# Optimization experiments

Measured on AMD Instinct MI355X. Metric: run time of the kernel, lower is better.

## Reference

```python
import jax, jax.numpy as jnp
import numpy as np

P, Q, R, H1, H2, PH, B = 32, 32, 8, 128, 64, 16, 8192
PAIRS = P * Q
OUT = PAIRS * R  # X_Z_layer output units


def _pairwise_mask(p, q, r):
    # rows i*q+k correspond to pair (x_i, z_k): connected to x_i and z_k only
    mx = np.zeros((p * q, p), np.float32)
    for i in range(p):
        mx[i * q:(i + 1) * q, i] = 1.0
    mz = np.tile(np.eye(q, dtype=np.float32), (p, 1))
    m = np.concatenate([mx, mz], axis=1)          # [p*q, p+q]
    return np.repeat(m, r, axis=0)                 # [p*q*r, p+q]


def setup_inputs() -> dict:
    key = jax.random.key(0)
    ks = jax.random.split(key, 24)
    rn = lambda k, s, sc=0.1: jax.random.normal(k, s, jnp.float32) * sc
    x = jax.random.normal(ks[0], (B, P), jnp.float32)
    z = jax.random.normal(ks[1], (B, Q), jnp.float32)
    # X_mlp: P -> H1 -> H2 -> 1
    xw1, xb1 = rn(ks[2], (P, H1)), rn(ks[3], (H1,))
    xw2, xb2 = rn(ks[4], (H1, H2)), rn(ks[5], (H2,))
    xw3, xb3 = rn(ks[6], (H2, 1)), rn(ks[7], (1,))
    # Z_mlp: Q -> H1 -> H2 -> 1
    zw1, zb1 = rn(ks[8], (Q, H1)), rn(ks[9], (H1,))
    zw2, zb2 = rn(ks[10], (Q if False else H1, H2)), rn(ks[11], (H2,))
    zw3, zb3 = rn(ks[12], (H2, 1)), rn(ks[13], (1,))
    # masked X_Z_layer: weight pre-multiplied by structured mask (as in __init__)
    mask = jnp.asarray(_pairwise_mask(P, Q, R))    # [OUT, P+Q]
    xzw = (rn(ks[14], (OUT, P + Q)) * mask).T      # [P+Q, OUT]
    xzb = rn(ks[15], (OUT,))
    # 1024 tiny per-pair MLPs: R -> PH (bias) -> 1 (no bias), stacked
    pw1 = rn(ks[16], (PAIRS, R, PH))
    pb1 = rn(ks[17], (PAIRS, PH))
    pw2 = rn(ks[18], (PAIRS, PH))
    return dict(x=x, z=z, xw1=xw1, xb1=xb1, xw2=xw2, xb2=xb2, xw3=xw3, xb3=xb3,
                zw1=zw1, zb1=zb1, zw2=zw2, zb2=zb2, zw3=zw3, zb3=zb3,
                xzw=xzw, xzb=xzb, pw1=pw1, pb1=pb1, pw2=pw2)


def reference(x, z, xw1, xb1, xw2, xb2, xw3, xb3,
              zw1, zb1, zw2, zb2, zw3, zb3, xzw, xzb, pw1, pb1, pw2):
    relu = jax.nn.relu
    # main-effect MLPs
    hx = relu(relu(x @ xw1 + xb1) @ xw2 + xb2)
    out_x = hx @ xw3 + xb3                         # [B,1]
    hz = relu(relu(z @ zw1 + zb1) @ zw2 + zb2)
    out_z = hz @ zw3 + zb3                         # [B,1]
    # masked interaction layer
    xz = jnp.concatenate([x, z], axis=1)           # [B, P+Q]
    h = relu(xz @ xzw + xzb)                       # [B, OUT]
    # all 1024 per-pair MLPs as one batched GEMM
    hp = h.reshape(h.shape[0], PAIRS, R)           # [B, pairs, R]
    t = relu(jnp.einsum('bpr,prh->bph', hp, pw1) + pb1)
    out_xz = jnp.einsum('bph,ph->b', t, pw2)[:, None]  # sum over pairs -> [B,1]
    return out_x + out_z + out_xz
```

## Files before the change

### kernel.cpp

```cpp
#include <hip/hip_runtime.h>

#define B_TOT 8192
#define PP 32
#define QQ 32
#define RR 8
#define H1 128
#define H2 64
#define PHH 16
#define PAIRS 1024
#define OUT_UNITS 8192

#define NBLK_IA 4096
#define NBLK_MM 512

typedef float f32x16 __attribute__((ext_vector_type(16)));
typedef short s16x8  __attribute__((ext_vector_type(8)));

union FragU { s16x8 v; unsigned int u[4]; };

__device__ inline unsigned int pack_bf16(float lo, float hi) {
    return __builtin_amdgcn_perm(__float_as_uint(hi), __float_as_uint(lo), 0x07060302u);
}

union SharedU {
    struct {
        float zT[16][128];
        float4 lwx[16][2];
        float4 lwz[16][2];
        float4 lhb[16][2];
        unsigned lpw1[16][4][16];
        float lpb[16][16];
        float lpw2[16][16];
        float red[128][33];
    } ia;
    struct {
        float h1T[128][65];
        float red2[4][64];
    } mm;
};

__global__ __launch_bounds__(256, 4) void fused_k(
    const float* __restrict__ x, const float* __restrict__ z,
    const float* __restrict__ xw1, const float* __restrict__ xb1,
    const float* __restrict__ xw2, const float* __restrict__ xb2,
    const float* __restrict__ xw3, const float* __restrict__ xb3,
    const float* __restrict__ zw1, const float* __restrict__ zb1,
    const float* __restrict__ zw2, const float* __restrict__ zb2,
    const float* __restrict__ zw3, const float* __restrict__ zb3,
    const float* __restrict__ xzw, const float* __restrict__ xzb,
    const float* __restrict__ pw1, const float* __restrict__ pb1,
    const float* __restrict__ pw2, float* __restrict__ out)
{
    __shared__ SharedU sh;
    const int bid  = blockIdx.x;
    const int t    = threadIdx.x;
    const int w    = t >> 6;
    const int lane = t & 63;

    if (bid < NBLK_IA) {
        const int bx    = bid & 63;
        const int y     = bid >> 6;
        const int m     = lane & 31;
        const int kh    = lane >> 5;
        const int jj    = m & 15;
        const int cph   = m >> 4;
        const int b0    = bx * 128;
        const int i_x   = y >> 1;
        const int k0    = (y & 1) * 16;
        const int pair0 = y * 16;

        {
            int row = t >> 1;
            int c8  = (t & 1) * 8;
            const float* src = z + (size_t)(b0 + row) * 32 + k0 + c8;
            float4 a4 = *reinterpret_cast<const float4*>(src);
            float4 b4 = *reinterpret_cast<const float4*>(src + 4);
            sh.ia.zT[c8+0][row] = a4.x; sh.ia.zT[c8+1][row] = a4.y;
            sh.ia.zT[c8+2][row] = a4.z; sh.ia.zT[c8+3][row] = a4.w;
            sh.ia.zT[c8+4][row] = b4.x; sh.ia.zT[c8+5][row] = b4.y;
            sh.ia.zT[c8+6][row] = b4.z; sh.ia.zT[c8+7][row] = b4.w;
        }
        if (t < 128) {
            int p = t >> 3, c = t & 7;
            int gp = pair0 + p;
            reinterpret_cast<float*>(sh.ia.lwx)[t] = xzw[(size_t)i_x * OUT_UNITS + gp*8 + c];
            reinterpret_cast<float*>(sh.ia.lwz)[t] = xzw[(size_t)(32 + k0 + p) * OUT_UNITS + gp*8 + c];
            reinterpret_cast<float*>(sh.ia.lhb)[t] = xzb[gp*8 + c];
        }
        {
            int p = t >> 4, j = t & 15;
            int gp = pair0 + p;
            sh.ia.lpb[p][j]  = pb1[gp*PHH + j];
            sh.ia.lpw2[p][j] = pw2[gp*PHH + j];
        }
        #pragma unroll
        for (int it = 0; it < 4; ++it) {
            int idx = t + it * 256;
            int p = idx >> 6, u = (idx >> 4) & 3, j = idx & 15;
            int gp = pair0 + p;
            float lo = pw1[(size_t)gp * 128 + (2*u)*16 + j];
            float hi = pw1[(size_t)gp * 128 + (2*u+1)*16 + j];
            sh.ia.lpw1[p][u][j] = pack_bf16(lo, hi);
        }

        const int bl = (w & 1) * 64 + m;
        const float xv0 = x[(size_t)(b0 + bl)      * 32 + i_x];
        const float xv1 = x[(size_t)(b0 + bl + 32) * 32 + i_x];
        __syncthreads();

        f32x16 acc0, acc1;
        #pragma unroll
        for (int r = 0; r < 16; ++r) { acc0[r] = 0.f; acc1[r] = 0.f; }

        const bool realB = (kh == cph);
        const int  ppl0  = (w >> 1) * 4;

        #pragma unroll 2
        for (int kk = 0; kk < 4; ++kk) {
            const int ppl = ppl0 + kk;
            const int pAl = 2*ppl + kh;
            const int pBl = 2*ppl + cph;

            const float zv0 = sh.ia.zT[pAl][bl];
            const float zv1 = sh.ia.zT[pAl][bl + 32];
            const float4 wxa = sh.ia.lwx[pAl][0], wxb = sh.ia.lwx[pAl][1];
            const float4 wza = sh.ia.lwz[pAl][0], wzb = sh.ia.lwz[pAl][1];
            const float4 hba = sh.ia.lhb[pAl][0], hbb = sh.ia.lhb[pAl][1];

            float h0[8], h1v[8];
            h0[0] = fmaxf(fmaf(xv0, wxa.x, fmaf(zv0, wza.x, hba.x)), 0.f);
            h0[1] = fmaxf(fmaf(xv0, wxa.y, fmaf(zv0, wza.y, hba.y)), 0.f);
            h0[2] = fmaxf(fmaf(xv0, wxa.z, fmaf(zv0, wza.z, hba.z)), 0.f);
            h0[3] = fmaxf(fmaf(xv0, wxa.w, fmaf(zv0, wza.w, hba.w)), 0.f);
            h0[4] = fmaxf(fmaf(xv0, wxb.x, fmaf(zv0, wzb.x, hbb.x)), 0.f);
            h0[5] = fmaxf(fmaf(xv0, wxb.y, fmaf(zv0, wzb.y, hbb.y)), 0.f);
            h0[6] = fmaxf(fmaf(xv0, wxb.z, fmaf(zv0, wzb.z, hbb.z)), 0.f);
            h0[7] = fmaxf(fmaf(xv0, wxb.w, fmaf(zv0, wzb.w, hbb.w)), 0.f);
            h1v[0] = fmaxf(fmaf(xv1, wxa.x, fmaf(zv1, wza.x, hba.x)), 0.f);
            h1v[1] = fmaxf(fmaf(xv1, wxa.y, fmaf(zv1, wza.y, hba.y)), 0.f);
            h1v[2] = fmaxf(fmaf(xv1, wxa.z, fmaf(zv1, wza.z, hba.z)), 0.f);
            h1v[3] = fmaxf(fmaf(xv1, wxa.w, fmaf(zv1, wza.w, hba.w)), 0.f);
            h1v[4] = fmaxf(fmaf(xv1, wxb.x, fmaf(zv1, wzb.x, hbb.x)), 0.f);
            h1v[5] = fmaxf(fmaf(xv1, wxb.y, fmaf(zv1, wzb.y, hbb.y)), 0.f);
            h1v[6] = fmaxf(fmaf(xv1, wxb.z, fmaf(zv1, wzb.z, hbb.z)), 0.f);
            h1v[7] = fmaxf(fmaf(xv1, wxb.w, fmaf(zv1, wzb.w, hbb.w)), 0.f);

            FragU a0, a1, bf;
            a0.u[0] = pack_bf16(h0[0], h0[1]);
            a0.u[1] = pack_bf16(h0[2], h0[3]);
            a0.u[2] = pack_bf16(h0[4], h0[5]);
            a0.u[3] = pack_bf16(h0[6], h0[7]);
            a1.u[0] = pack_bf16(h1v[0], h1v[1]);
            a1.u[1] = pack_bf16(h1v[2], h1v[3]);
            a1.u[2] = pack_bf16(h1v[4], h1v[5]);
            a1.u[3] = pack_bf16(h1v[6], h1v[7]);
            bf.u[0] = realB ? sh.ia.lpw1[pBl][0][jj] : 0u;
            bf.u[1] = realB ? sh.ia.lpw1[pBl][1][jj] : 0u;
            bf.u[2] = realB ? sh.ia.lpw1[pBl][2][jj] : 0u;
            bf.u[3] = realB ? sh.ia.lpw1[pBl][3][jj] : 0u;

            const float pbv = sh.ia.lpb[pBl][jj];
            const float w2v = sh.ia.lpw2[pBl][jj];

            f32x16 cpb;
            #pragma unroll
            for (int r = 0; r < 16; ++r) cpb[r] = pbv;

            f32x16 d0 = __builtin_amdgcn_mfma_f32_32x32x16_bf16(a0.v, bf.v, cpb, 0, 0, 0);
            f32x16 d1 = __builtin_amdgcn_mfma_f32_32x32x16_bf16(a1.v, bf.v, cpb, 0, 0, 0);

            #pragma unroll
            for (int r = 0; r < 16; ++r)
                acc0[r] = fmaf(fmaxf(d0[r], 0.f), w2v, acc0[r]);
            #pragma unroll
            for (int r = 0; r < 16; ++r)
                acc1[r] = fmaf(fmaxf(d1[r], 0.f), w2v, acc1[r]);
        }

        const int rb0 = (w & 1) * 64;
        if (w < 2) {
            #pragma unroll
            for (int r = 0; r < 16; ++r) {
                int rowf = (r & 3) + 8 * (r >> 2) + 4 * kh;
                sh.ia.red[rb0 + rowf][m]      = acc0[r];
                sh.ia.red[rb0 + 32 + rowf][m] = acc1[r];
            }
        }
        __syncthreads();
        if (w >= 2) {
            #pragma unroll
            for (int r = 0; r < 16; ++r) {
                int rowf = (r & 3) + 8 * (r >> 2) + 4 * kh;
                sh.ia.red[rb0 + rowf][m]      += acc0[r];
                sh.ia.red[rb0 + 32 + rowf][m] += acc1[r];
            }
        }
        __syncthreads();
        if (t < 128) {
            float s = 0.f;
            #pragma unroll
            for (int c = 0; c < 32; ++c) s += sh.ia.red[t][c];
            atomicAdd(out + b0 + t, s);
        }
    } else {
        const int r2    = bid - NBLK_IA;
        const int btile = r2 & 127;
        const int hf    = (r2 >> 7) & 1;
        const int which = (r2 >> 8) & 1;
        const float* in = which ? z   : x;
        const float* w1 = which ? zw1 : xw1;
        const float* b1 = which ? zb1 : xb1;
        const float* w2 = which ? zw2 : xw2;
        const float* b2 = which ? zb2 : xb2;
        const float* w3 = which ? zw3 : xw3;
        const float* b3 = which ? zb3 : xb3;

        const int wu = __builtin_amdgcn_readfirstlane(w);
        const int b0 = btile * 64;

        float xr[32];
        const float4* xrp = reinterpret_cast<const float4*>(in + (size_t)(b0 + lane) * 32);
        #pragma unroll
        for (int q = 0; q < 8; ++q) {
            float4 v = xrp[q];
            xr[4*q] = v.x; xr[4*q+1] = v.y; xr[4*q+2] = v.z; xr[4*q+3] = v.w;
        }

        float h1[32];
        #pragma unroll
        for (int j = 0; j < 32; ++j) h1[j] = b1[wu*32 + j];
        #pragma unroll
        for (int mm = 0; mm < 32; ++mm) {
            float xv = xr[mm];
            #pragma unroll
            for (int j = 0; j < 32; ++j)
                h1[j] = fmaf(xv, w1[mm*H1 + wu*32 + j], h1[j]);
        }
        #pragma unroll
        for (int j = 0; j < 32; ++j)
            sh.mm.h1T[wu*32 + j][lane] = fmaxf(h1[j], 0.f);
        __syncthreads();

        const int n0 = __builtin_amdgcn_readfirstlane(hf*32 + wu*8);
        float h2[8];
        #pragma unroll
        for (int n = 0; n < 8; ++n) h2[n] = b2[n0 + n];
        #pragma unroll 4
        for (int mm = 0; mm < 128; ++mm) {
            float hv = sh.mm.h1T[mm][lane];
            #pragma unroll
            for (int n = 0; n < 8; ++n)
                h2[n] = fmaf(hv, w2[mm*H2 + n0 + n], h2[n]);
        }
        float p = 0.f;
        #pragma unroll
        for (int n = 0; n < 8; ++n)
            p = fmaf(fmaxf(h2[n], 0.f), w3[n0 + n], p);

        sh.mm.red2[wu][lane] = p;
        __syncthreads();
        if (wu == 0) {
            float s = sh.mm.red2[0][lane] + sh.mm.red2[1][lane]
                    + sh.mm.red2[2][lane] + sh.mm.red2[3][lane];
            if (hf == 0) s += b3[0];
            atomicAdd(out + b0 + lane, s);
        }
    }
}

extern "C" void kernel_launch(void* const* d_in, const int* in_sizes, int n_in,
                              void* d_out, int out_size, void* d_ws, size_t ws_size,
                              hipStream_t stream) {
    const float* x   = (const float*)d_in[0];
    const float* z   = (const float*)d_in[1];
    const float* xw1 = (const float*)d_in[2];
    const float* xb1 = (const float*)d_in[3];
    const float* xw2 = (const float*)d_in[4];
    const float* xb2 = (const float*)d_in[5];
    const float* xw3 = (const float*)d_in[6];
    const float* xb3 = (const float*)d_in[7];
    const float* zw1 = (const float*)d_in[8];
    const float* zb1 = (const float*)d_in[9];
    const float* zw2 = (const float*)d_in[10];
    const float* zb2 = (const float*)d_in[11];
    const float* zw3 = (const float*)d_in[12];
    const float* zb3 = (const float*)d_in[13];
    const float* xzw = (const float*)d_in[14];
    const float* xzb = (const float*)d_in[15];
    const float* pw1 = (const float*)d_in[16];
    const float* pb1 = (const float*)d_in[17];
    const float* pw2 = (const float*)d_in[18];
    float* out = (float*)d_out;

    hipMemsetAsync(out, 0, (size_t)out_size * sizeof(float), stream);

    fused_k<<<dim3(NBLK_IA + NBLK_MM), 256, 0, stream>>>(
        x, z, xw1, xb1, xw2, xb2, xw3, xb3,
        zw1, zb1, zw2, zb2, zw3, zb3,
        xzw, xzb, pw1, pb1, pw2, out);
}
```

Baseline: 137.4 us.

## Shrink shared memory footprint and raise occupancy; schedule MLP blocks first

The interaction-stage reduction buffer now overlays the staging arrays through a nested union, with an extra barrier before the overlay is written. The main-effect MLP path computes its hidden layer in two halves of 64 units, halving the h1T buffer and the h1 register array. Launch bounds rise from 4 to 6 blocks per SM so that smaller LDS and register use can allow more resident blocks. The heavier MLP blocks move to the low block indices so they are dispatched first rather than trailing at the tail. The changes add extra barriers and risk register pressure or spills under the tighter launch bound.

```diff
diff --git a/kernel.cpp b/kernel.cpp
--- a/kernel.cpp
+++ b/kernel.cpp
@@ -23,23 +23,25 @@
 }
 
 union SharedU {
-    struct {
-        float zT[16][128];
-        float4 lwx[16][2];
-        float4 lwz[16][2];
-        float4 lhb[16][2];
-        unsigned lpw1[16][4][16];
-        float lpb[16][16];
-        float lpw2[16][16];
+    union {
+        struct {
+            float zT[16][128];
+            float4 lwx[16][2];
+            float4 lwz[16][2];
+            float4 lhb[16][2];
+            unsigned lpw1[16][4][16];
+            float lpb[16][16];
+            float lpw2[16][16];
+        } s;
         float red[128][33];
     } ia;
     struct {
-        float h1T[128][65];
+        float h1T[64][65];
         float red2[4][64];
     } mm;
 };
 
-__global__ __launch_bounds__(256, 4) void fused_k(
+__global__ __launch_bounds__(256, 6) void fused_k(
     const float* __restrict__ x, const float* __restrict__ z,
     const float* __restrict__ xw1, const float* __restrict__ xb1,
     const float* __restrict__ xw2, const float* __restrict__ xb2,
@@ -57,9 +59,10 @@
     const int w    = t >> 6;
     const int lane = t & 63;
 
-    if (bid < NBLK_IA) {
-        const int bx    = bid & 63;
-        const int y     = bid >> 6;
+    if (bid >= NBLK_MM) {
+        const int ib    = bid - NBLK_MM;
+        const int bx    = ib & 63;
+        const int y     = ib >> 6;
         const int m     = lane & 31;
         const int kh    = lane >> 5;
         const int jj    = m & 15;
@@ -75,23 +78,23 @@
             const float* src = z + (size_t)(b0 + row) * 32 + k0 + c8;
             float4 a4 = *reinterpret_cast<const float4*>(src);
             float4 b4 = *reinterpret_cast<const float4*>(src + 4);
-            sh.ia.zT[c8+0][row] = a4.x; sh.ia.zT[c8+1][row] = a4.y;
-            sh.ia.zT[c8+2][row] = a4.z; sh.ia.zT[c8+3][row] = a4.w;
-            sh.ia.zT[c8+4][row] = b4.x; sh.ia.zT[c8+5][row] = b4.y;
-            sh.ia.zT[c8+6][row] = b4.z; sh.ia.zT[c8+7][row] = b4.w;
+            sh.ia.s.zT[c8+0][row] = a4.x; sh.ia.s.zT[c8+1][row] = a4.y;
+            sh.ia.s.zT[c8+2][row] = a4.z; sh.ia.s.zT[c8+3][row] = a4.w;
+            sh.ia.s.zT[c8+4][row] = b4.x; sh.ia.s.zT[c8+5][row] = b4.y;
+            sh.ia.s.zT[c8+6][row] = b4.z; sh.ia.s.zT[c8+7][row] = b4.w;
         }
         if (t < 128) {
             int p = t >> 3, c = t & 7;
             int gp = pair0 + p;
-            reinterpret_cast<float*>(sh.ia.lwx)[t] = xzw[(size_t)i_x * OUT_UNITS + gp*8 + c];
-            reinterpret_cast<float*>(sh.ia.lwz)[t] = xzw[(size_t)(32 + k0 + p) * OUT_UNITS + gp*8 + c];
-            reinterpret_cast<float*>(sh.ia.lhb)[t] = xzb[gp*8 + c];
+            reinterpret_cast<float*>(sh.ia.s.lwx)[t] = xzw[(size_t)i_x * OUT_UNITS + gp*8 + c];
+            reinterpret_cast<float*>(sh.ia.s.lwz)[t] = xzw[(size_t)(32 + k0 + p) * OUT_UNITS + gp*8 + c];
+            reinterpret_cast<float*>(sh.ia.s.lhb)[t] = xzb[gp*8 + c];
         }
         {
             int p = t >> 4, j = t & 15;
             int gp = pair0 + p;
-            sh.ia.lpb[p][j]  = pb1[gp*PHH + j];
-            sh.ia.lpw2[p][j] = pw2[gp*PHH + j];
+            sh.ia.s.lpb[p][j]  = pb1[gp*PHH + j];
+            sh.ia.s.lpw2[p][j] = pw2[gp*PHH + j];
         }
         #pragma unroll
         for (int it = 0; it < 4; ++it) {
@@ -100,7 +103,7 @@
             int gp = pair0 + p;
             float lo = pw1[(size_t)gp * 128 + (2*u)*16 + j];
             float hi = pw1[(size_t)gp * 128 + (2*u+1)*16 + j];
-            sh.ia.lpw1[p][u][j] = pack_bf16(lo, hi);
+            sh.ia.s.lpw1[p][u][j] = pack_bf16(lo, hi);
         }
 
         const int bl = (w & 1) * 64 + m;
@@ -121,11 +124,11 @@
             const int pAl = 2*ppl + kh;
             const int pBl = 2*ppl + cph;
 
-            const float zv0 = sh.ia.zT[pAl][bl];
-            const float zv1 = sh.ia.zT[pAl][bl + 32];
-            const float4 wxa = sh.ia.lwx[pAl][0], wxb = sh.ia.lwx[pAl][1];
-            const float4 wza = sh.ia.lwz[pAl][0], wzb = sh.ia.lwz[pAl][1];
-            const float4 hba = sh.ia.lhb[pAl][0], hbb = sh.ia.lhb[pAl][1];
+            const float zv0 = sh.ia.s.zT[pAl][bl];
+            const float zv1 = sh.ia.s.zT[pAl][bl + 32];
+            const float4 wxa = sh.ia.s.lwx[pAl][0], wxb = sh.ia.s.lwx[pAl][1];
+            const float4 wza = sh.ia.s.lwz[pAl][0], wzb = sh.ia.s.lwz[pAl][1];
+            const float4 hba = sh.ia.s.lhb[pAl][0], hbb = sh.ia.s.lhb[pAl][1];
 
             float h0[8], h1v[8];
             h0[0] = fmaxf(fmaf(xv0, wxa.x, fmaf(zv0, wza.x, hba.x)), 0.f);
@@ -154,13 +157,13 @@
             a1.u[1] = pack_bf16(h1v[2], h1v[3]);
             a1.u[2] = pack_bf16(h1v[4], h1v[5]);
             a1.u[3] = pack_bf16(h1v[6], h1v[7]);
-            bf.u[0] = realB ? sh.ia.lpw1[pBl][0][jj] : 0u;
-            bf.u[1] = realB ? sh.ia.lpw1[pBl][1][jj] : 0u;
-            bf.u[2] = realB ? sh.ia.lpw1[pBl][2][jj] : 0u;
-            bf.u[3] = realB ? sh.ia.lpw1[pBl][3][jj] : 0u;
-
-            const float pbv = sh.ia.lpb[pBl][jj];
-            const float w2v = sh.ia.lpw2[pBl][jj];
+            bf.u[0] = realB ? sh.ia.s.lpw1[pBl][0][jj] : 0u;
+            bf.u[1] = realB ? sh.ia.s.lpw1[pBl][1][jj] : 0u;
+            bf.u[2] = realB ? sh.ia.s.lpw1[pBl][2][jj] : 0u;
+            bf.u[3] = realB ? sh.ia.s.lpw1[pBl][3][jj] : 0u;
+
+            const float pbv = sh.ia.s.lpb[pBl][jj];
+            const float w2v = sh.ia.s.lpw2[pBl][jj];
 
             f32x16 cpb;
             #pragma unroll
@@ -177,6 +180,7 @@
                 acc1[r] = fmaf(fmaxf(d1[r], 0.f), w2v, acc1[r]);
         }
 
+        __syncthreads();
         const int rb0 = (w & 1) * 64;
         if (w < 2) {
             #pragma unroll
@@ -203,7 +207,7 @@
             atomicAdd(out + b0 + t, s);
         }
     } else {
-        const int r2    = bid - NBLK_IA;
+        const int r2    = bid;
         const int btile = r2 & 127;
         const int hf    = (r2 >> 7) & 1;
         const int which = (r2 >> 8) & 1;
@@ -226,31 +230,36 @@
             xr[4*q] = v.x; xr[4*q+1] = v.y; xr[4*q+2] = v.z; xr[4*q+3] = v.w;
         }
 
-        float h1[32];
-        #pragma unroll
-        for (int j = 0; j < 32; ++j) h1[j] = b1[wu*32 + j];
-        #pragma unroll
-        for (int mm = 0; mm < 32; ++mm) {
-            float xv = xr[mm];
-            #pragma unroll
-            for (int j = 0; j < 32; ++j)
-                h1[j] = fmaf(xv, w1[mm*H1 + wu*32 + j], h1[j]);
-        }
-        #pragma unroll
-        for (int j = 0; j < 32; ++j)
-            sh.mm.h1T[wu*32 + j][lane] = fmaxf(h1[j], 0.f);
-        __syncthreads();
-
         const int n0 = __builtin_amdgcn_readfirstlane(hf*32 + wu*8);
         float h2[8];
         #pragma unroll
         for (int n = 0; n < 8; ++n) h2[n] = b2[n0 + n];
-        #pragma unroll 4
-        for (int mm = 0; mm < 128; ++mm) {
-            float hv = sh.mm.h1T[mm][lane];
-            #pragma unroll
-            for (int n = 0; n < 8; ++n)
-                h2[n] = fmaf(hv, w2[mm*H2 + n0 + n], h2[n]);
+
+        #pragma unroll
+        for (int half = 0; half < 2; ++half) {
+            const int j0 = half*64 + wu*16;
+            float h1[16];
+            #pragma unroll
+            for (int j = 0; j < 16; ++j) h1[j] = b1[j0 + j];
+            #pragma unroll
+            for (int mm = 0; mm < 32; ++mm) {
+                float xv = xr[mm];
+                #pragma unroll
+                for (int j = 0; j < 16; ++j)
+                    h1[j] = fmaf(xv, w1[mm*H1 + j0 + j], h1[j]);
+            }
+            __syncthreads();
+            #pragma unroll
+            for (int j = 0; j < 16; ++j)
+                sh.mm.h1T[wu*16 + j][lane] = fmaxf(h1[j], 0.f);
+            __syncthreads();
+            #pragma unroll 4
+            for (int mm = 0; mm < 64; ++mm) {
+                float hv = sh.mm.h1T[mm][lane];
+                #pragma unroll
+                for (int n = 0; n < 8; ++n)
+                    h2[n] = fmaf(hv, w2[(half*64 + mm)*H2 + n0 + n], h2[n]);
+            }
         }
         float p = 0.f;
         #pragma unroll
```

New measurement: 205.0 us. +49.2%, slower.
